# Optimization experiments

Hardware: AMD Instinct MI355X
Metric: run time of the kernel (lower is better)

The kernel has to match this reference:

```python
import jax, jax.numpy as jnp
import numpy as np

N, C, H, K = 4096, 512, 128, 3
NEG = -jnp.inf


def _linear(x, W, b):
    return x @ W.T + b


def _lrelu(x):
    return jnp.where(x > 0, x, 0.01 * x)  # nn.LeakyReLU default slope


def _cos_sim(x, y):
    # torch cal_cos_similarity: xy / (|x| |y|^T), NaN (0/0) -> 0
    xy = x @ y.T
    den = jnp.linalg.norm(x, axis=1, keepdims=True) * jnp.linalg.norm(y, axis=1, keepdims=True).T
    return xy / jnp.where(den == 0, 1.0, den)


def setup_inputs() -> dict:
    key = jax.random.key(0)
    ks = jax.random.split(key, 24)
    x_hidden = jax.random.normal(ks[0], (N, H), jnp.float32)
    cm = (jax.random.uniform(ks[1], (N, C)) < 0.05).astype(jnp.float32)
    # ensure every concept has at least one member stock (no empty concepts)
    cm = cm.at[jnp.arange(C) % N, jnp.arange(C)].set(1.0)
    market_value = jax.random.uniform(ks[2], (N,), jnp.float32, 0.1, 1.0)
    s = 1.0 / np.sqrt(H)
    inp = {"x_hidden": x_hidden, "concept_matrix": cm, "market_value": market_value}
    names = ["ps", "ps_fore", "ps_back", "hs", "hs_fore", "hs_back", "indi"]
    for i, n in enumerate(names):
        inp[f"W_{n}"] = jax.random.uniform(ks[3 + 2 * i], (H, H), jnp.float32, -s, s)
        inp[f"b_{n}"] = jax.random.uniform(ks[4 + 2 * i], (H,), jnp.float32, -s, s)
    inp["W_out"] = jax.random.uniform(ks[20], (1, H), jnp.float32, -s, s)
    inp["b_out"] = jax.random.uniform(ks[21], (1,), jnp.float32, -s, s)
    return inp


def reference(x_hidden, concept_matrix, market_value,
              W_ps, b_ps, W_ps_fore, b_ps_fore, W_ps_back, b_ps_back,
              W_hs, b_hs, W_hs_fore, b_hs_fore, W_hs_back, b_hs_back,
              W_indi, b_indi, W_out, b_out):
    x = x_hidden
    n = x.shape[0]
    # --- predefined-concept (ps) branch ---
    s2c = concept_matrix * market_value[:, None]                     # [N,C]
    s2c_den = s2c.sum(0)[None, :] * concept_matrix + 1.0
    s2c = s2c / s2c_den
    hidden = s2c.T @ x                                               # [C,H]
    valid1 = hidden.sum(1) != 0                                      # row-filter mask
    s2c2 = jax.nn.softmax(x @ hidden.T, axis=0)                      # softmax over stocks
    hidden = (s2c2.T @ x) * valid1[:, None]                          # [C,H]
    c2s = jax.nn.softmax(jnp.where(valid1[None, :], _cos_sim(x, hidden), NEG), axis=1)
    p_shared = _linear(c2s @ hidden, W_ps, b_ps)
    p_back = _linear(p_shared, W_ps_back, b_ps_back)
    out_ps = _lrelu(_linear(p_shared, W_ps_fore, b_ps_fore))
    # --- hidden-concept (hs) branch ---
    h = x - p_back
    hs2c = _cos_sim(h, h)                                            # [N,N]
    diag = jnp.diagonal(hs2c)
    hs2c = hs2c * (1.0 - jnp.eye(n, dtype=h.dtype))
    idx = jax.lax.top_k(hs2c, K)[1]                                  # [N,K]
    mask = jnp.zeros((n, n), h.dtype).at[jnp.arange(n)[:, None], idx].set(1.0)
    hs2c = hs2c * mask
    hs2c = hs2c + jnp.diag((hs2c.sum(0) != 0).astype(h.dtype) * diag)
    hidden2 = hs2c.T @ h                                             # [N,H]
    valid2 = hidden2.sum(1) != 0
    hidden2 = hidden2 * valid2[:, None]
    hc2s = jax.nn.softmax(jnp.where(valid2[None, :], _cos_sim(h, hidden2), NEG), axis=1)
    h_shared = _linear(hc2s @ hidden2, W_hs, b_hs)
    h_back = _linear(h_shared, W_hs_back, b_hs_back)
    out_hs = _lrelu(_linear(h_shared, W_hs_fore, b_hs_fore))
    # --- individual branch ---
    indiv = x - p_back - h_back
    out_indi = _lrelu(_linear(indiv, W_indi, b_indi))
    all_info = out_ps + out_hs + out_indi
    return _linear(all_info, W_out, b_out).squeeze()                 # [N]
```

## Files before the change

### kernel.cpp

```cpp
#include <hip/hip_runtime.h>
#include <hip/hip_fp16.h>
#include <math.h>

#define N 4096
#define C 512
#define H 128
#define PAD 40
#define WP 136
#define FWP 136
#define SP 136

typedef __attribute__((ext_vector_type(8))) short bf16x8;
typedef __attribute__((ext_vector_type(4))) float f32x4;


__device__ inline float wave_reduce_sum(float v) {
#pragma unroll
  for (int m = 32; m; m >>= 1) v += __shfl_xor(v, m);
  return v;
}

__device__ inline float lrelu(float v) { return v > 0.f ? v : 0.01f * v; }

__device__ inline bool better(float v, int j, float w, int k) {
  return (v > w) || (v == w && j < k);
}

__device__ inline void top3_ins(float v, int j, float& v0, int& j0,
                                float& v1, int& j1, float& v2, int& j2) {
  if (better(v, j, v0, j0)) { v2 = v1; j2 = j1; v1 = v0; j1 = j0; v0 = v; j0 = j; }
  else if (better(v, j, v1, j1)) { v2 = v1; j2 = j1; v1 = v; j1 = j; }
  else if (better(v, j, v2, j2)) { v2 = v; j2 = j; }
}

__device__ inline void ins5(float s, int j, float v[5], int jx[5]) {
  if (!better(s, j, v[4], jx[4])) return;
  if (better(s, j, v[0], jx[0])) {
    v[4]=v[3]; jx[4]=jx[3]; v[3]=v[2]; jx[3]=jx[2]; v[2]=v[1]; jx[2]=jx[1];
    v[1]=v[0]; jx[1]=jx[0]; v[0]=s; jx[0]=j;
  } else if (better(s, j, v[1], jx[1])) {
    v[4]=v[3]; jx[4]=jx[3]; v[3]=v[2]; jx[3]=jx[2]; v[2]=v[1]; jx[2]=jx[1];
    v[1]=s; jx[1]=j;
  } else if (better(s, j, v[2], jx[2])) {
    v[4]=v[3]; jx[4]=jx[3]; v[3]=v[2]; jx[3]=jx[2]; v[2]=s; jx[2]=j;
  } else if (better(s, j, v[3], jx[3])) {
    v[4]=v[3]; jx[4]=jx[3]; v[3]=s; jx[3]=j;
  } else {
    v[4]=s; jx[4]=j;
  }
}

__device__ inline unsigned short f2bf(float f) {
  unsigned u = __float_as_uint(f);
  unsigned r = u + 0x7fffu + ((u >> 16) & 1u);
  return (unsigned short)(r >> 16);
}
__device__ inline float bf2f(unsigned short h) {
  return __uint_as_float(((unsigned)h) << 16);
}

__global__ __launch_bounds__(256) void k_split(const float* __restrict__ in,
                                               unsigned short* __restrict__ hi,
                                               unsigned short* __restrict__ lo,
                                               float* __restrict__ nrm) {
  int t = threadIdx.x;
  int idx = (blockIdx.x * 256 + t) * 4;
  float4 v = *(const float4*)&in[idx];
  float vv[4] = {v.x, v.y, v.z, v.w};
  unsigned short h[4], l[4];
  float ss = 0.f;
#pragma unroll
  for (int c = 0; c < 4; c++) {
    ss += vv[c] * vv[c];
    h[c] = f2bf(vv[c]);
    l[c] = f2bf(vv[c] - bf2f(h[c]));
  }
  uint2 ph = {(unsigned)h[0] | ((unsigned)h[1] << 16),
              (unsigned)h[2] | ((unsigned)h[3] << 16)};
  uint2 pl = {(unsigned)l[0] | ((unsigned)l[1] << 16),
              (unsigned)l[2] | ((unsigned)l[3] << 16)};
  *(uint2*)&hi[idx] = ph;
  *(uint2*)&lo[idx] = pl;
  if (nrm) {
#pragma unroll
    for (int m = 16; m; m >>= 1) ss += __shfl_xor(ss, m);
    if ((t & 31) == 0) nrm[idx >> 7] = sqrtf(ss);
  }
}

__global__ __launch_bounds__(256) void k_tsplit(const float* __restrict__ in,
                                                unsigned short* __restrict__ thi,
                                                unsigned short* __restrict__ tlo,
                                                int R) {
  __shared__ float tile[32][132];
  int r0 = blockIdx.x * 32, tid = threadIdx.x;
#pragma unroll
  for (int q = 0; q < 4; q++) {
    int f = q * 256 + tid;
    int row = f >> 5, ch = f & 31;
    *(float4*)&tile[row][ch * 4] = *(const float4*)&in[(size_t)(r0 + row) * 128 + ch * 4];
  }
  __syncthreads();
  int c = tid & 127, half = tid >> 7;
  unsigned short hh[16], ll[16];
#pragma unroll
  for (int rr = 0; rr < 16; rr++) {
    float v = tile[half * 16 + rr][c];
    hh[rr] = f2bf(v);
    ll[rr] = f2bf(v - bf2f(hh[rr]));
  }
  size_t off = (size_t)c * R + r0 + half * 16;
  uint4 ph0 = {(unsigned)hh[0] | ((unsigned)hh[1] << 16), (unsigned)hh[2] | ((unsigned)hh[3] << 16),
               (unsigned)hh[4] | ((unsigned)hh[5] << 16), (unsigned)hh[6] | ((unsigned)hh[7] << 16)};
  uint4 ph1 = {(unsigned)hh[8] | ((unsigned)hh[9] << 16), (unsigned)hh[10] | ((unsigned)hh[11] << 16),
               (unsigned)hh[12] | ((unsigned)hh[13] << 16), (unsigned)hh[14] | ((unsigned)hh[15] << 16)};
  uint4 pl0 = {(unsigned)ll[0] | ((unsigned)ll[1] << 16), (unsigned)ll[2] | ((unsigned)ll[3] << 16),
               (unsigned)ll[4] | ((unsigned)ll[5] << 16), (unsigned)ll[6] | ((unsigned)ll[7] << 16)};
  uint4 pl1 = {(unsigned)ll[8] | ((unsigned)ll[9] << 16), (unsigned)ll[10] | ((unsigned)ll[11] << 16),
               (unsigned)ll[12] | ((unsigned)ll[13] << 16), (unsigned)ll[14] | ((unsigned)ll[15] << 16)};
  *(uint4*)&thi[off] = ph0; *(uint4*)&thi[off + 8] = ph1;
  *(uint4*)&tlo[off] = pl0; *(uint4*)&tlo[off + 8] = pl1;
}


__global__ __launch_bounds__(64) void k_colsum_s2c(
    const float* __restrict__ cm, const float* __restrict__ mv,
    float* __restrict__ colsum_c) {
  int c = blockIdx.x * 64 + threadIdx.x;
  int i0 = blockIdx.y * 256;
  float acc = 0.f;
  for (int i = i0; i < i0 + 256; i++) acc += cm[(size_t)i * C + c] * mv[i];
  atomicAdd(&colsum_c[c], acc);
}

__global__ __launch_bounds__(256) void k_colstats(const float* __restrict__ sc,
                                                  float* __restrict__ colmax,
                                                  float* __restrict__ colsum) {
  __shared__ float red[256];
  int c = blockIdx.x, t = threadIdx.x;
  float v[16];
  float m = -3e38f;
#pragma unroll
  for (int q = 0; q < 16; q++) {
    v[q] = sc[(size_t)(q * 256 + t) * C + c];
    m = fmaxf(m, v[q]);
  }
  red[t] = m; __syncthreads();
  for (int s = 128; s; s >>= 1) { if (t < s) red[t] = fmaxf(red[t], red[t + s]); __syncthreads(); }
  m = red[0]; __syncthreads();
  float sum = 0.f;
#pragma unroll
  for (int q = 0; q < 16; q++) sum += __expf(v[q] - m);
  red[t] = sum; __syncthreads();
  for (int s = 128; s; s >>= 1) { if (t < s) red[t] += red[t + s]; __syncthreads(); }
  if (t == 0) { colmax[c] = m; colsum[c] = red[0]; }
}

__global__ __launch_bounds__(256) void k_cs_softmax(
    const float* __restrict__ sc, const float* __restrict__ xnorm,
    const float* __restrict__ hnorm, const float* __restrict__ valid1,
    unsigned short* __restrict__ cshi, unsigned short* __restrict__ cslo) {
  __shared__ float red[256];
  int i = blockIdx.x, t = threadIdx.x;
  float xn = xnorm[i];
  float r0 = sc[(size_t)i * C + t], r1 = sc[(size_t)i * C + 256 + t];
  float d0 = xn * hnorm[t], d1 = xn * hnorm[256 + t];
  float c0 = r0 / (d0 == 0.f ? 1.f : d0);
  float c1 = r1 / (d1 == 0.f ? 1.f : d1);
  float s0 = (valid1[t] != 0.f) ? c0 : -3e38f;
  float s1 = (valid1[256 + t] != 0.f) ? c1 : -3e38f;
  red[t] = fmaxf(s0, s1); __syncthreads();
  for (int s = 128; s; s >>= 1) { if (t < s) red[t] = fmaxf(red[t], red[t + s]); __syncthreads(); }
  float m = red[0]; __syncthreads();
  float p0 = (s0 > -1e37f) ? __expf(s0 - m) : 0.f;
  float p1 = (s1 > -1e37f) ? __expf(s1 - m) : 0.f;
  red[t] = p0 + p1; __syncthreads();
  for (int s = 128; s; s >>= 1) { if (t < s) red[t] += red[t + s]; __syncthreads(); }
  float inv = 1.f / red[0];
  float a = p0 * inv, b = p1 * inv;
  unsigned short ha = f2bf(a), hb = f2bf(b);
  cshi[(size_t)i * C + t] = ha;
  cslo[(size_t)i * C + t] = f2bf(a - bf2f(ha));
  cshi[(size_t)i * C + 256 + t] = hb;
  cslo[(size_t)i * C + 256 + t] = f2bf(b - bf2f(hb));
}

__global__ __launch_bounds__(64) void k_fin_hidden2(
    const float* __restrict__ h, const float* __restrict__ diagv,
    const float* __restrict__ colsum_m, float* __restrict__ hidden2,
    unsigned short* __restrict__ h2hi, unsigned short* __restrict__ h2lo,
    float* __restrict__ valid2f) {
  int j = blockIdx.x, t = threadIdx.x;
  float add = (colsum_m[j] != 0.f) ? diagv[j] : 0.f;
  float a = hidden2[(size_t)j * H + t] + add * h[(size_t)j * H + t];
  float b = hidden2[(size_t)j * H + 64 + t] + add * h[(size_t)j * H + 64 + t];
  float s = a + b, ss = a * a + b * b;
#pragma unroll
  for (int m = 32; m; m >>= 1) { s += __shfl_xor(s, m); ss += __shfl_xor(ss, m); }
  bool valid = (s != 0.f);
  a = valid ? a : 0.f; b = valid ? b : 0.f;
  hidden2[(size_t)j * H + t] = a;
  hidden2[(size_t)j * H + 64 + t] = b;
  float inv = (valid && ss > 0.f) ? (1.f / sqrtf(ss)) : 1.f;
  float va = a * inv, vb = b * inv;
  unsigned short ha = f2bf(va), hb = f2bf(vb);
  h2hi[(size_t)j * H + t] = ha;
  h2lo[(size_t)j * H + t] = f2bf(va - bf2f(ha));
  h2hi[(size_t)j * H + 64 + t] = hb;
  h2lo[(size_t)j * H + 64 + t] = f2bf(vb - bf2f(hb));
  if (t == 0) valid2f[j] = valid ? 1.f : 0.f;
}

template <int EPI>
__global__ __launch_bounds__(256) void k_mfma_nt(
    const unsigned short* __restrict__ Ahi, const unsigned short* __restrict__ Alo,
    const unsigned short* __restrict__ Bhi, const unsigned short* __restrict__ Blo,
    float* __restrict__ out, float2* __restrict__ cand, int Nn) {
  __shared__ __align__(16) unsigned short sAh[128 * PAD];
  __shared__ __align__(16) unsigned short sAl[128 * PAD];
  __shared__ __align__(16) unsigned short sBh[128 * PAD];
  __shared__ __align__(16) unsigned short sBl[128 * PAD];
  int tid = threadIdx.x;
  int bm = blockIdx.y * 128, bn = blockIdx.x * 128;
  int lane = tid & 63, w = tid >> 6;
  int wm = (w & 1) * 64, wn = (w >> 1) * 64;
  int l15 = lane & 15, quad = lane >> 4;
  f32x4 zero = {0.f, 0.f, 0.f, 0.f};
  f32x4 acc[4][4];
#pragma unroll
  for (int mt = 0; mt < 4; mt++)
#pragma unroll
    for (int nt = 0; nt < 4; nt++) acc[mt][nt] = zero;

  for (int kt = 0; kt < 128; kt += 32) {
#pragma unroll
    for (int q = 0; q < 2; q++) {
      int f = tid * 2 + q;
      int row = f >> 2, ch = f & 3;
      size_t ga = (size_t)(bm + row) * 128 + kt + ch * 8;
      size_t gb = (size_t)(bn + row) * 128 + kt + ch * 8;
      int ls = row * PAD + ch * 8;
      *(uint4*)&sAh[ls] = *(const uint4*)&Ahi[ga];
      *(uint4*)&sAl[ls] = *(const uint4*)&Alo[ga];
      *(uint4*)&sBh[ls] = *(const uint4*)&Bhi[gb];
      *(uint4*)&sBl[ls] = *(const uint4*)&Blo[gb];
    }
    __syncthreads();
    bf16x8 ah[4], al[4], bh[4], bl[4];
#pragma unroll
    for (int t = 0; t < 4; t++) {
      int ar = (wm + t * 16 + l15) * PAD + quad * 8;
      ah[t] = *(const bf16x8*)&sAh[ar];
      al[t] = *(const bf16x8*)&sAl[ar];
      int br = (wn + t * 16 + l15) * PAD + quad * 8;
      bh[t] = *(const bf16x8*)&sBh[br];
      bl[t] = *(const bf16x8*)&sBl[br];
    }
#pragma unroll
    for (int mt = 0; mt < 4; mt++)
#pragma unroll
      for (int nt = 0; nt < 4; nt++) {
        acc[mt][nt] = __builtin_amdgcn_mfma_f32_16x16x32_bf16(ah[mt], bh[nt], acc[mt][nt], 0, 0, 0);
        acc[mt][nt] = __builtin_amdgcn_mfma_f32_16x16x32_bf16(ah[mt], bl[nt], acc[mt][nt], 0, 0, 0);
        acc[mt][nt] = __builtin_amdgcn_mfma_f32_16x16x32_bf16(al[mt], bh[nt], acc[mt][nt], 0, 0, 0);
      }
    __syncthreads();
  }
  if constexpr (EPI == 2) {
    __shared__ __align__(16) unsigned short sS[128 * SP];
#pragma unroll
    for (int mt = 0; mt < 4; mt++)
#pragma unroll
      for (int nt = 0; nt < 4; nt++) {
        int coll = wn + nt * 16 + l15;
#pragma unroll
        for (int rg = 0; rg < 4; rg++) {
          int rowl = wm + mt * 16 + quad * 4 + rg;
          float v = (bm + rowl == bn + coll) ? 0.f : acc[mt][nt][rg];
          sS[rowl * SP + coll] = __half_as_ushort(__float2half(v));
        }
      }
    __syncthreads();
    int r = tid >> 1, hf = tid & 1;
    const unsigned short* rowp = &sS[r * SP + hf * 64];
    int cbase = bn + hf * 64;
    float v5[5] = {-3e38f, -3e38f, -3e38f, -3e38f, -3e38f};
    int j5[5] = {0x7fffffff, 0x7fffffff, 0x7fffffff, 0x7fffffff, 0x7fffffff};
#pragma unroll
    for (int q = 0; q < 8; q++) {
      uint4 p = *(const uint4*)&rowp[q * 8];
      unsigned pk[4] = {p.x, p.y, p.z, p.w};
#pragma unroll
      for (int c2 = 0; c2 < 4; c2++) {
        float e0 = __half2float(__ushort_as_half((unsigned short)(pk[c2] & 0xffffu)));
        float e1 = __half2float(__ushort_as_half((unsigned short)(pk[c2] >> 16)));
        ins5(e0, cbase + q * 8 + c2 * 2, v5, j5);
        ins5(e1, cbase + q * 8 + c2 * 2 + 1, v5, j5);
      }
    }
    int slot = (bn >> 6) + hf;
    float2* cp = &cand[((size_t)(bm + r) * 64 + slot) * 5];
#pragma unroll
    for (int c2 = 0; c2 < 5; c2++) cp[c2] = {v5[c2], __int_as_float(j5[c2])};
  } else {
#pragma unroll
    for (int mt = 0; mt < 4; mt++) {
#pragma unroll
      for (int nt = 0; nt < 4; nt++) {
        int col = bn + wn + nt * 16 + l15;
#pragma unroll
        for (int rg = 0; rg < 4; rg++) {
          int row = bm + wm + mt * 16 + quad * 4 + rg;
          out[(size_t)row * Nn + col] = acc[mt][nt][rg];
        }
      }
    }
  }
}

__global__ __launch_bounds__(256) void k_rowtop2(
    const float2* __restrict__ cand, const float* __restrict__ hhat,
    float* __restrict__ mtv, int* __restrict__ mtj) {
  int i = blockIdx.x * 4 + (threadIdx.x >> 6);
  int lane = threadIdx.x & 63;
  const float2* cr = &cand[(size_t)i * 320];
  float v[5] = {-3e38f, -3e38f, -3e38f, -3e38f, -3e38f};
  int jx[5] = {0x7fffffff, 0x7fffffff, 0x7fffffff, 0x7fffffff, 0x7fffffff};
#pragma unroll
  for (int c = 0; c < 5; c++) {
    float2 p = cr[lane * 5 + c];
    ins5(p.x, __float_as_int(p.y), v, jx);
  }
#pragma unroll
  for (int d = 1; d < 64; d <<= 1) {
    float fv[5]; int fj[5];
#pragma unroll
    for (int c = 0; c < 5; c++) { fv[c] = __shfl_xor(v[c], d); fj[c] = __shfl_xor(jx[c], d); }
#pragma unroll
    for (int c = 0; c < 5; c++) ins5(fv[c], fj[c], v, jx);
  }
  const float* hi = &hhat[(size_t)i * H];
  float b0 = -3e38f, b1 = -3e38f, b2 = -3e38f;
  int q0 = 0, q1 = 0, q2 = 0;
#pragma unroll
  for (int c = 0; c < 5; c++) {
    int j = jx[c];
    float s;
    if (j == i) {
      s = 0.f;
    } else {
      const float* hj = &hhat[(size_t)j * H];
      float p = hi[lane] * hj[lane] + hi[lane + 64] * hj[lane + 64];
      s = wave_reduce_sum(p);
    }
    top3_ins(s, j, b0, q0, b1, q1, b2, q2);
  }
  if (lane == 0) {
    mtv[i * 3 + 0] = b0; mtv[i * 3 + 1] = b1; mtv[i * 3 + 2] = b2;
    mtj[i * 3 + 0] = q0; mtj[i * 3 + 1] = q1; mtj[i * 3 + 2] = q2;
  }
}

__global__ __launch_bounds__(512) void k_flash(
    const unsigned short* __restrict__ Qhi, const unsigned short* __restrict__ Qlo,
    const unsigned short* __restrict__ Khi, const unsigned short* __restrict__ Klo,
    const unsigned short* __restrict__ Vthi, const unsigned short* __restrict__ Vtlo,
    const float* __restrict__ valid2f, float* __restrict__ partialU,
    float* __restrict__ plsum, int KVC) {
  __shared__ __align__(16) unsigned short sQh[128 * FWP];
  __shared__ __align__(16) unsigned short sQl[128 * FWP];
  __shared__ __align__(16) unsigned short sP[128 * FWP];
  __shared__ __align__(16) unsigned short sKh[128 * PAD];
  __shared__ __align__(16) unsigned short sKl[128 * PAD];
  __shared__ __align__(16) unsigned short sVh[128 * PAD];
  __shared__ __align__(16) unsigned short sVl[128 * PAD];
  __shared__ float lsum_s[128];
  int tid = threadIdx.x;
  int z = blockIdx.x;
  int bm = blockIdx.y * 128;
  int j0 = z * KVC;
  int lane = tid & 63, w = tid >> 6;
  int wm = (w & 3) * 32, wn = (w >> 2) * 64;
  int l15 = lane & 15, quad = lane >> 4;
#pragma unroll
  for (int q = 0; q < 4; q++) {
    int f = q * 512 + tid;
    int row = f >> 4, ch = f & 15;
    size_t ga = (size_t)(bm + row) * 128 + ch * 8;
    int ls = row * FWP + ch * 8;
    *(uint4*)&sQh[ls] = *(const uint4*)&Qhi[ga];
    *(uint4*)&sQl[ls] = *(const uint4*)&Qlo[ga];
  }
  if (tid < 128) lsum_s[tid] = 0.f;
  __syncthreads();
  f32x4 zero = {0.f, 0.f, 0.f, 0.f};
  f32x4 uacc[2][4];
#pragma unroll
  for (int mt = 0; mt < 2; mt++)
#pragma unroll
    for (int nt = 0; nt < 4; nt++) uacc[mt][nt] = zero;

  for (int jb = j0; jb < j0 + KVC; jb += 128) {
    float vm[4];
#pragma unroll
    for (int nt = 0; nt < 4; nt++) vm[nt] = valid2f[jb + wn + nt * 16 + l15];
    f32x4 qacc[2][4];
#pragma unroll
    for (int mt = 0; mt < 2; mt++)
#pragma unroll
      for (int nt = 0; nt < 4; nt++) qacc[mt][nt] = zero;
    for (int kt = 0; kt < 128; kt += 32) {
      {
        int row = tid >> 2, ch = tid & 3;
        size_t gb = (size_t)(jb + row) * 128 + kt + ch * 8;
        int ls = row * PAD + ch * 8;
        *(uint4*)&sKh[ls] = *(const uint4*)&Khi[gb];
        *(uint4*)&sKl[ls] = *(const uint4*)&Klo[gb];
      }
      __syncthreads();
      bf16x8 ah[2], al[2], bh[4], bl[4];
#pragma unroll
      for (int t = 0; t < 2; t++) {
        int ar = (wm + t * 16 + l15) * FWP + kt + quad * 8;
        ah[t] = *(const bf16x8*)&sQh[ar];
        al[t] = *(const bf16x8*)&sQl[ar];
      }
#pragma unroll
      for (int t = 0; t < 4; t++) {
        int br = (wn + t * 16 + l15) * PAD + quad * 8;
        bh[t] = *(const bf16x8*)&sKh[br];
        bl[t] = *(const bf16x8*)&sKl[br];
      }
#pragma unroll
      for (int mt = 0; mt < 2; mt++)
#pragma unroll
        for (int nt = 0; nt < 4; nt++) {
          qacc[mt][nt] = __builtin_amdgcn_mfma_f32_16x16x32_bf16(ah[mt], bh[nt], qacc[mt][nt], 0, 0, 0);
          qacc[mt][nt] = __builtin_amdgcn_mfma_f32_16x16x32_bf16(ah[mt], bl[nt], qacc[mt][nt], 0, 0, 0);
          qacc[mt][nt] = __builtin_amdgcn_mfma_f32_16x16x32_bf16(al[mt], bh[nt], qacc[mt][nt], 0, 0, 0);
        }
      __syncthreads();
    }
#pragma unroll
    for (int mt = 0; mt < 2; mt++) {
#pragma unroll
      for (int rg = 0; rg < 4; rg++) {
        int row = wm + mt * 16 + quad * 4 + rg;
        float rs = 0.f;
#pragma unroll
        for (int nt = 0; nt < 4; nt++) {
          float e = (vm[nt] != 0.f) ? __expf(qacc[mt][nt][rg] - 1.f) : 0.f;
          rs += e;
          sP[row * FWP + wn + nt * 16 + l15] = f2bf(e);
        }
#pragma unroll
        for (int d = 1; d < 16; d <<= 1) rs += __shfl_xor(rs, d);
        if (l15 == 0) atomicAdd(&lsum_s[row], rs);
      }
    }
    for (int kt = 0; kt < 128; kt += 32) {
      {
        int row = tid >> 2, ch = tid & 3;
        size_t gv = (size_t)row * N + jb + kt + ch * 8;
        int ls = row * PAD + ch * 8;
        *(uint4*)&sVh[ls] = *(const uint4*)&Vthi[gv];
        *(uint4*)&sVl[ls] = *(const uint4*)&Vtlo[gv];
      }
      __syncthreads();
      bf16x8 pa[2], vh[4], vl[4];
#pragma unroll
      for (int t = 0; t < 2; t++) {
        int ar = (wm + t * 16 + l15) * FWP + kt + quad * 8;
        pa[t] = *(const bf16x8*)&sP[ar];
      }
#pragma unroll
      for (int t = 0; t < 4; t++) {
        int br = (wn + t * 16 + l15) * PAD + quad * 8;
        vh[t] = *(const bf16x8*)&sVh[br];
        vl[t] = *(const bf16x8*)&sVl[br];
      }
#pragma unroll
      for (int mt = 0; mt < 2; mt++)
#pragma unroll
        for (int nt = 0; nt < 4; nt++) {
          uacc[mt][nt] = __builtin_amdgcn_mfma_f32_16x16x32_bf16(pa[mt], vh[nt], uacc[mt][nt], 0, 0, 0);
          uacc[mt][nt] = __builtin_amdgcn_mfma_f32_16x16x32_bf16(pa[mt], vl[nt], uacc[mt][nt], 0, 0, 0);
        }
      __syncthreads();
    }
  }
  float* pU = partialU + (size_t)z * N * 128;
#pragma unroll
  for (int mt = 0; mt < 2; mt++)
#pragma unroll
    for (int nt = 0; nt < 4; nt++) {
      int col = wn + nt * 16 + l15;
#pragma unroll
      for (int rg = 0; rg < 4; rg++) {
        int row = bm + wm + mt * 16 + quad * 4 + rg;
        pU[(size_t)row * 128 + col] = uacc[mt][nt][rg];
      }
    }
  if (tid < 128) plsum[(size_t)z * N + bm + tid] = lsum_s[tid];
}

__global__ __launch_bounds__(256) void k_mfma_kn(
    const unsigned short* __restrict__ Ahi, const unsigned short* __restrict__ Alo,
    const unsigned short* __restrict__ Bthi, const unsigned short* __restrict__ Btlo,
    float* __restrict__ partial, int lda, int KC) {
  __shared__ __align__(16) unsigned short sAh[128 * PAD];
  __shared__ __align__(16) unsigned short sAl[128 * PAD];
  __shared__ __align__(16) unsigned short sBh[128 * PAD];
  __shared__ __align__(16) unsigned short sBl[128 * PAD];
  int tid = threadIdx.x;
  int bm = blockIdx.y * 128;
  int k0 = blockIdx.z * KC;
  int lane = tid & 63, w = tid >> 6;
  int wm = (w & 1) * 64, wn = (w >> 1) * 64;
  int l15 = lane & 15, quad = lane >> 4;
  f32x4 zero = {0.f, 0.f, 0.f, 0.f};
  f32x4 acc[4][4];
#pragma unroll
  for (int mt = 0; mt < 4; mt++)
#pragma unroll
    for (int nt = 0; nt < 4; nt++) acc[mt][nt] = zero;

  for (int kt = 0; kt < KC; kt += 32) {
#pragma unroll
    for (int q = 0; q < 2; q++) {
      int f = tid * 2 + q;
      int row = f >> 2, ch = f & 3;
      size_t ga = (size_t)(bm + row) * lda + k0 + kt + ch * 8;
      size_t gb = (size_t)row * lda + k0 + kt + ch * 8;
      int ls = row * PAD + ch * 8;
      *(uint4*)&sAh[ls] = *(const uint4*)&Ahi[ga];
      *(uint4*)&sAl[ls] = *(const uint4*)&Alo[ga];
      *(uint4*)&sBh[ls] = *(const uint4*)&Bthi[gb];
      *(uint4*)&sBl[ls] = *(const uint4*)&Btlo[gb];
    }
    __syncthreads();
    bf16x8 ah[4], al[4], bh[4], bl[4];
#pragma unroll
    for (int t = 0; t < 4; t++) {
      int ar = (wm + t * 16 + l15) * PAD + quad * 8;
      ah[t] = *(const bf16x8*)&sAh[ar];
      al[t] = *(const bf16x8*)&sAl[ar];
      int br = (wn + t * 16 + l15) * PAD + quad * 8;
      bh[t] = *(const bf16x8*)&sBh[br];
      bl[t] = *(const bf16x8*)&sBl[br];
    }
#pragma unroll
    for (int mt = 0; mt < 4; mt++)
#pragma unroll
      for (int nt = 0; nt < 4; nt++) {
        acc[mt][nt] = __builtin_amdgcn_mfma_f32_16x16x32_bf16(ah[mt], bh[nt], acc[mt][nt], 0, 0, 0);
        acc[mt][nt] = __builtin_amdgcn_mfma_f32_16x16x32_bf16(ah[mt], bl[nt], acc[mt][nt], 0, 0, 0);
        acc[mt][nt] = __builtin_amdgcn_mfma_f32_16x16x32_bf16(al[mt], bh[nt], acc[mt][nt], 0, 0, 0);
      }
    __syncthreads();
  }
  float* pp = partial + (size_t)blockIdx.z * N * 128;
#pragma unroll
  for (int mt = 0; mt < 4; mt++)
#pragma unroll
    for (int nt = 0; nt < 4; nt++) {
      int col = wn + nt * 16 + l15;
#pragma unroll
      for (int rg = 0; rg < 4; rg++) {
        int row = bm + wm + mt * 16 + quad * 4 + rg;
        pp[(size_t)row * 128 + col] = acc[mt][nt][rg];
      }
    }
}

template <int AMODE>
__global__ __launch_bounds__(256) void k_mfma_genA(
    const float* __restrict__ P, const float* __restrict__ mv,
    const float* __restrict__ col1, const float* __restrict__ col2,
    const unsigned short* __restrict__ Bthi, const unsigned short* __restrict__ Btlo,
    float* __restrict__ partial, int KC) {
  __shared__ __align__(16) unsigned short sAh[128 * PAD];
  __shared__ __align__(16) unsigned short sAl[128 * PAD];
  __shared__ __align__(16) unsigned short sBh[128 * PAD];
  __shared__ __align__(16) unsigned short sBl[128 * PAD];
  int tid = threadIdx.x;
  int bm = blockIdx.y * 128;
  int k0 = blockIdx.z * KC;
  int lane = tid & 63, w = tid >> 6;
  int wm = (w & 1) * 64, wn = (w >> 1) * 64;
  int l15 = lane & 15, quad = lane >> 4;
  f32x4 zero = {0.f, 0.f, 0.f, 0.f};
  f32x4 acc[4][4];
#pragma unroll
  for (int mt = 0; mt < 4; mt++)
#pragma unroll
    for (int nt = 0; nt < 4; nt++) acc[mt][nt] = zero;

  for (int kt = 0; kt < KC; kt += 32) {
    int kr = tid >> 3;
    int mc = (tid & 7) * 16;
    int k = k0 + kt + kr;
    float mvk = (AMODE == 1) ? mv[k] : 0.f;
#pragma unroll
    for (int q = 0; q < 4; q++) {
      int m0 = mc + q * 4;
      float4 pv = *(const float4*)&P[(size_t)k * C + bm + m0];
      float4 c1 = *(const float4*)&col1[bm + m0];
      float wv[4];
      if (AMODE == 1) {
        wv[0] = pv.x * mvk / (c1.x * pv.x + 1.f);
        wv[1] = pv.y * mvk / (c1.y * pv.y + 1.f);
        wv[2] = pv.z * mvk / (c1.z * pv.z + 1.f);
        wv[3] = pv.w * mvk / (c1.w * pv.w + 1.f);
      } else {
        float4 c2 = *(const float4*)&col2[bm + m0];
        wv[0] = __expf(pv.x - c1.x) / c2.x;
        wv[1] = __expf(pv.y - c1.y) / c2.y;
        wv[2] = __expf(pv.z - c1.z) / c2.z;
        wv[3] = __expf(pv.w - c1.w) / c2.w;
      }
#pragma unroll
      for (int j = 0; j < 4; j++) {
        unsigned short hh = f2bf(wv[j]);
        sAh[(m0 + j) * PAD + kr] = hh;
        sAl[(m0 + j) * PAD + kr] = f2bf(wv[j] - bf2f(hh));
      }
    }
#pragma unroll
    for (int q = 0; q < 2; q++) {
      int f = q * 256 + tid;
      int row = f >> 2, ch = f & 3;
      size_t gb = (size_t)row * N + k0 + kt + ch * 8;
      int ls = row * PAD + ch * 8;
// ... 150 lines not shown
  __shared__ __align__(16) unsigned short sAh[32 * WP];
  __shared__ __align__(16) unsigned short sAl[32 * WP];
  __shared__ __align__(16) float sF[32][132];
  int tid = threadIdx.x;
  int bm = blockIdx.x * 32;
  int lane = tid & 63, w = tid >> 6;
  int rt = (w & 1) * 16, ch2 = (w >> 1) * 64;
  int l15 = lane & 15, quad = lane >> 4;
  f32x4 zero = {0.f, 0.f, 0.f, 0.f};
  f32x4 acc[4];

  {
    int row = tid >> 3, c0 = (tid & 7) * 16;
    const float* src = &A[(size_t)(bm + row) * 128 + c0];
#pragma unroll
    for (int q = 0; q < 4; q++) {
      float4 v = *(const float4*)&src[q * 4];
      float vv[4] = {v.x, v.y, v.z, v.w};
#pragma unroll
      for (int c = 0; c < 4; c++) {
        unsigned short hh = f2bf(vv[c]);
        sAh[row * WP + c0 + q * 4 + c] = hh;
        sAl[row * WP + c0 + q * 4 + c] = f2bf(vv[c] - bf2f(hh));
      }
    }
  }
  LOAD_W(W_ps);
  __syncthreads();
  GEMM32(acc);
  __syncthreads();
#pragma unroll
  for (int nt = 0; nt < 4; nt++) {
    int col = ch2 + nt * 16 + l15;
    float bv = b_ps[col];
#pragma unroll
    for (int rg = 0; rg < 4; rg++) {
      int row = rt + quad * 4 + rg;
      float v = acc[nt][rg] + bv;
      unsigned short hh = f2bf(v);
      sAh[row * WP + col] = hh;
      sAl[row * WP + col] = f2bf(v - bf2f(hh));
    }
  }
  LOAD_W(W_psb);
  __syncthreads();
  GEMM32(acc);
#pragma unroll
  for (int nt = 0; nt < 4; nt++) {
    int col = ch2 + nt * 16 + l15;
    float bv = b_psb[col];
#pragma unroll
    for (int rg = 0; rg < 4; rg++) {
      int row = rt + quad * 4 + rg;
      size_t off = (size_t)(bm + row) * 128 + col;
      float hv = x[off] - (acc[nt][rg] + bv);
      hbuf[off] = hv;
      sF[row][col] = hv;
    }
  }
  __syncthreads();
  {
    int row = tid >> 3, c0 = (tid & 7) * 16;
    float hv16[16];
    float ssp = 0.f;
#pragma unroll
    for (int q = 0; q < 16; q++) {
      float v = sF[row][c0 + q];
      hv16[q] = v;
      ssp += v * v;
    }
    ssp += __shfl_xor(ssp, 1);
    ssp += __shfl_xor(ssp, 2);
    ssp += __shfl_xor(ssp, 4);
    float ss = ssp;
    float hn = sqrtf(ss);
    float den = hn * hn;
    float dg = (den == 0.f) ? 0.f : ss / den;
    float inv = (ss > 0.f) ? (1.f / hn) : 1.f;
    size_t base = (size_t)(bm + row) * H + c0;
    float va16[16];
    unsigned short hh16[16], ll16[16];
#pragma unroll
    for (int q = 0; q < 16; q++) {
      va16[q] = hv16[q] * inv;
      hh16[q] = f2bf(va16[q]);
      ll16[q] = f2bf(va16[q] - bf2f(hh16[q]));
    }
#pragma unroll
    for (int q4 = 0; q4 < 4; q4++) {
      float4 fv = {va16[q4 * 4], va16[q4 * 4 + 1], va16[q4 * 4 + 2], va16[q4 * 4 + 3]};
      *(float4*)&hhat[base + q4 * 4] = fv;
    }
    uint4 ph0 = {(unsigned)hh16[0] | ((unsigned)hh16[1] << 16), (unsigned)hh16[2] | ((unsigned)hh16[3] << 16),
                 (unsigned)hh16[4] | ((unsigned)hh16[5] << 16), (unsigned)hh16[6] | ((unsigned)hh16[7] << 16)};
    uint4 ph1 = {(unsigned)hh16[8] | ((unsigned)hh16[9] << 16), (unsigned)hh16[10] | ((unsigned)hh16[11] << 16),
                 (unsigned)hh16[12] | ((unsigned)hh16[13] << 16), (unsigned)hh16[14] | ((unsigned)hh16[15] << 16)};
    uint4 pl0 = {(unsigned)ll16[0] | ((unsigned)ll16[1] << 16), (unsigned)ll16[2] | ((unsigned)ll16[3] << 16),
                 (unsigned)ll16[4] | ((unsigned)ll16[5] << 16), (unsigned)ll16[6] | ((unsigned)ll16[7] << 16)};
    uint4 pl1 = {(unsigned)ll16[8] | ((unsigned)ll16[9] << 16), (unsigned)ll16[10] | ((unsigned)ll16[11] << 16),
                 (unsigned)ll16[12] | ((unsigned)ll16[13] << 16), (unsigned)ll16[14] | ((unsigned)ll16[15] << 16)};
    *(uint4*)&hhi[base] = ph0; *(uint4*)&hhi[base + 8] = ph1;
    *(uint4*)&hlo[base] = pl0; *(uint4*)&hlo[base + 8] = pl1;
    if ((tid & 7) == 0) diagv[bm + row] = dg;
  }
  LOAD_W(W_psf);
  __syncthreads();
  GEMM32(acc);
#pragma unroll
  for (int nt = 0; nt < 4; nt++) {
    int col = ch2 + nt * 16 + l15;
    float bv = b_psf[col];
#pragma unroll
    for (int rg = 0; rg < 4; rg++) {
      int row = rt + quad * 4 + rg;
      size_t off = (size_t)(bm + row) * 128 + col;
      all_info[off] = lrelu(acc[nt][rg] + bv);
    }
  }
}

__global__ __launch_bounds__(256) void k_hs_tail(
    const float* __restrict__ A, const float* __restrict__ hbuf,
    const float* __restrict__ all_info,
    const float* __restrict__ W_hs, const float* __restrict__ b_hs,
    const float* __restrict__ W_hsf, const float* __restrict__ b_hsf,
    const float* __restrict__ W_hsb, const float* __restrict__ b_hsb,
    const float* __restrict__ W_in, const float* __restrict__ b_in,
    const float* __restrict__ W_out, const float* __restrict__ b_out,
    float* __restrict__ out) {
  __shared__ __align__(16) unsigned short sWh[128 * WP];
  __shared__ __align__(16) unsigned short sWl[128 * WP];
  __shared__ __align__(16) unsigned short sAh[32 * WP];
  __shared__ __align__(16) unsigned short sAl[32 * WP];
  __shared__ __align__(16) float sF[32][132];
  int tid = threadIdx.x;
  int bm = blockIdx.x * 32;
  int lane = tid & 63, w = tid >> 6;
  int rt = (w & 1) * 16, ch2 = (w >> 1) * 64;
  int l15 = lane & 15, quad = lane >> 4;
  f32x4 zero = {0.f, 0.f, 0.f, 0.f};
  f32x4 acc[4];
  float allv[4][4];

  {
    int row = tid >> 3, c0 = (tid & 7) * 16;
    const float* src = &A[(size_t)(bm + row) * 128 + c0];
#pragma unroll
    for (int q = 0; q < 4; q++) {
      float4 v = *(const float4*)&src[q * 4];
      float vv[4] = {v.x, v.y, v.z, v.w};
#pragma unroll
      for (int c = 0; c < 4; c++) {
        unsigned short hh = f2bf(vv[c]);
        sAh[row * WP + c0 + q * 4 + c] = hh;
        sAl[row * WP + c0 + q * 4 + c] = f2bf(vv[c] - bf2f(hh));
      }
    }
  }
  LOAD_W(W_hs);
  __syncthreads();
  GEMM32(acc);
  __syncthreads();
#pragma unroll
  for (int nt = 0; nt < 4; nt++) {
    int col = ch2 + nt * 16 + l15;
    float bv = b_hs[col];
#pragma unroll
    for (int rg = 0; rg < 4; rg++) {
      int row = rt + quad * 4 + rg;
      float v = acc[nt][rg] + bv;
      unsigned short hh = f2bf(v);
      sAh[row * WP + col] = hh;
      sAl[row * WP + col] = f2bf(v - bf2f(hh));
    }
  }
  LOAD_W(W_hsf);
  __syncthreads();
  GEMM32(acc);
#pragma unroll
  for (int nt = 0; nt < 4; nt++) {
    int col = ch2 + nt * 16 + l15;
    float bv = b_hsf[col];
#pragma unroll
    for (int rg = 0; rg < 4; rg++) {
      int row = rt + quad * 4 + rg;
      size_t off = (size_t)(bm + row) * 128 + col;
      allv[nt][rg] = all_info[off] + lrelu(acc[nt][rg] + bv);
    }
  }
  __syncthreads();
  LOAD_W(W_hsb);
  __syncthreads();
  GEMM32(acc);
  float iv[4][4];
#pragma unroll
  for (int nt = 0; nt < 4; nt++) {
    int col = ch2 + nt * 16 + l15;
    float bv = b_hsb[col];
#pragma unroll
    for (int rg = 0; rg < 4; rg++) {
      int row = rt + quad * 4 + rg;
      size_t off = (size_t)(bm + row) * 128 + col;
      iv[nt][rg] = hbuf[off] - (acc[nt][rg] + bv);
    }
  }
  __syncthreads();
#pragma unroll
  for (int nt = 0; nt < 4; nt++) {
    int col = ch2 + nt * 16 + l15;
#pragma unroll
    for (int rg = 0; rg < 4; rg++) {
      int row = rt + quad * 4 + rg;
      unsigned short hh = f2bf(iv[nt][rg]);
      sAh[row * WP + col] = hh;
      sAl[row * WP + col] = f2bf(iv[nt][rg] - bf2f(hh));
    }
  }
  LOAD_W(W_in);
  __syncthreads();
  GEMM32(acc);
#pragma unroll
  for (int nt = 0; nt < 4; nt++) {
    int col = ch2 + nt * 16 + l15;
    float bv = b_in[col];
#pragma unroll
    for (int rg = 0; rg < 4; rg++) {
      int row = rt + quad * 4 + rg;
      allv[nt][rg] += lrelu(acc[nt][rg] + bv);
      sF[row][col] = allv[nt][rg];
    }
  }
  __syncthreads();
  {
    int row = tid >> 3, c0 = (tid & 7) * 16;
    float s = 0.f;
#pragma unroll
    for (int q = 0; q < 16; q++) s += sF[row][c0 + q] * W_out[c0 + q];
    s += __shfl_xor(s, 1);
    s += __shfl_xor(s, 2);
    s += __shfl_xor(s, 4);
    if ((tid & 7) == 0) out[bm + row] = s + b_out[0];
  }
}


extern "C" void kernel_launch(void* const* d_in, const int* in_sizes, int n_in,
                              void* d_out, int out_size, void* d_ws, size_t ws_size,
                              hipStream_t stream) {
  (void)in_sizes; (void)n_in; (void)out_size; (void)ws_size;
  const float* x   = (const float*)d_in[0];
  const float* cm  = (const float*)d_in[1];
  const float* mv  = (const float*)d_in[2];
  const float* W_ps = (const float*)d_in[3],  *b_ps = (const float*)d_in[4];
  const float* W_psf = (const float*)d_in[5], *b_psf = (const float*)d_in[6];
  const float* W_psb = (const float*)d_in[7], *b_psb = (const float*)d_in[8];
  const float* W_hs = (const float*)d_in[9],  *b_hs = (const float*)d_in[10];
  const float* W_hsf = (const float*)d_in[11], *b_hsf = (const float*)d_in[12];
  const float* W_hsb = (const float*)d_in[13], *b_hsb = (const float*)d_in[14];
  const float* W_in = (const float*)d_in[15], *b_in = (const float*)d_in[16];
  const float* W_out = (const float*)d_in[17], *b_out = (const float*)d_in[18];
  float* out = (float*)d_out;

  float* W = (float*)d_ws;
  size_t o = 0;
  auto alloc = [&](size_t n) { float* p = W + o; o += n; return p; };
  float* colsum_c = alloc(C);
  float* colmax   = alloc(C);
  float* colsumexp= alloc(C);
  float* valid1   = alloc(C);
  float* hnorm_ps = alloc(C);
  float* xnorm    = alloc(N);
  float* diagv    = alloc(N);
  float* colsum_m = alloc(N);
  float* valid2f  = alloc(N);
  float* plsum    = alloc((size_t)8 * N);
  float* mtv      = alloc(3 * N);
  int*   mtj      = (int*)alloc(3 * N);
  float* hidden1  = alloc((size_t)C * H);
  float* hidden_ps= alloc((size_t)C * H);
  float* scores   = alloc((size_t)N * C);
  float* ps_pre   = alloc((size_t)N * H);
  float* all_info = alloc((size_t)N * H);
  float* hbuf     = alloc((size_t)N * H);
  float* hhat     = alloc((size_t)N * H);
  float* hidden2  = alloc((size_t)N * H);
  unsigned short* xhi    = (unsigned short*)alloc((size_t)N * H / 2);
  unsigned short* xlo    = (unsigned short*)alloc((size_t)N * H / 2);
  unsigned short* hhathi = (unsigned short*)alloc((size_t)N * H / 2);
  unsigned short* hhatlo = (unsigned short*)alloc((size_t)N * H / 2);
  unsigned short* h2hi   = (unsigned short*)alloc((size_t)N * H / 2);
  unsigned short* h2lo   = (unsigned short*)alloc((size_t)N * H / 2);
  unsigned short* h1hi   = (unsigned short*)alloc((size_t)C * H / 2);
  unsigned short* h1lo   = (unsigned short*)alloc((size_t)C * H / 2);
  unsigned short* hpshi  = (unsigned short*)alloc((size_t)C * H / 2);
  unsigned short* hpslo  = (unsigned short*)alloc((size_t)C * H / 2);
  unsigned short* cshi   = (unsigned short*)alloc((size_t)N * C / 2);
  unsigned short* cslo   = (unsigned short*)alloc((size_t)N * C / 2);
  unsigned short* hpst_hi= (unsigned short*)alloc((size_t)H * C / 2);
  unsigned short* hpst_lo= (unsigned short*)alloc((size_t)H * C / 2);
  unsigned short* h2t_hi = (unsigned short*)alloc((size_t)H * N / 2);
  unsigned short* h2t_lo = (unsigned short*)alloc((size_t)H * N / 2);
  unsigned short* xt_hi  = (unsigned short*)alloc((size_t)H * N / 2);
  unsigned short* xt_lo  = (unsigned short*)alloc((size_t)H * N / 2);
  float2* cand    = (float2*)alloc((size_t)N * 64 * 5 * 2);
  float* partial  = W + o;
  const int Z = 8;

  hipMemsetAsync(colsum_c, 0, C * sizeof(float), stream);
  hipMemsetAsync(colsum_m, 0, N * sizeof(float), stream);
  hipMemsetAsync(hidden2, 0, (size_t)N * H * sizeof(float), stream);

  dim3 blk(256);
  k_split<<<dim3(N * H / 1024), blk, 0, stream>>>(x, xhi, xlo, xnorm);
  k_tsplit<<<dim3(N / 32), blk, 0, stream>>>(x, xt_hi, xt_lo, N);
  k_colsum_s2c<<<dim3(C / 64, 16), dim3(64), 0, stream>>>(cm, mv, colsum_c);
  k_mfma_genA<1><<<dim3(1, C / 128, 32), blk, 0, stream>>>(
      cm, mv, colsum_c, nullptr, xt_hi, xt_lo, partial, N / 32);
  k_reduce<<<dim3(C * H / 4 / 256), blk, 0, stream>>>(
      partial, hidden1, 32, (size_t)C * H, (size_t)C * H / 4, nullptr, nullptr,
      h1hi, h1lo, nullptr, valid1);
  k_mfma_nt<0><<<dim3(C / 128, N / 128), blk, 0, stream>>>(
      xhi, xlo, h1hi, h1lo, scores, nullptr, C);
  k_colstats<<<dim3(C), blk, 0, stream>>>(scores, colmax, colsumexp);
  k_mfma_genA<2><<<dim3(1, C / 128, 32), blk, 0, stream>>>(
      scores, nullptr, colmax, colsumexp, xt_hi, xt_lo, partial, N / 32);
  k_reduce<<<dim3(C * H / 4 / 256), blk, 0, stream>>>(
      partial, hidden_ps, 32, (size_t)C * H, (size_t)C * H / 4, valid1, nullptr,
      hpshi, hpslo, hnorm_ps, nullptr);
  k_mfma_nt<0><<<dim3(C / 128, N / 128), blk, 0, stream>>>(
      xhi, xlo, hpshi, hpslo, scores, nullptr, C);
  k_cs_softmax<<<dim3(N), blk, 0, stream>>>(scores, xnorm, hnorm_ps, valid1,
                                            cshi, cslo);
  k_tsplit<<<dim3(C / 32), blk, 0, stream>>>(hidden_ps, hpst_hi, hpst_lo, C);
  k_mfma_kn<<<dim3(1, N / 128, 4), blk, 0, stream>>>(
      cshi, cslo, hpst_hi, hpst_lo, partial, C, C / 4);
  k_reduce<<<dim3(N * H / 4 / 256), blk, 0, stream>>>(
      partial, ps_pre, 4, (size_t)N * H, (size_t)N * H / 4, nullptr, nullptr,
      nullptr, nullptr, nullptr, nullptr);
  k_ps_tail<<<dim3(N / 32), blk, 0, stream>>>(
      ps_pre, x, W_ps, b_ps, W_psb, b_psb, W_psf, b_psf,
      hbuf, hhat, hhathi, hhatlo, diagv, all_info);
  k_mfma_nt<2><<<dim3(N / 128, N / 128), blk, 0, stream>>>(
      hhathi, hhatlo, hhathi, hhatlo, nullptr, cand, N);
  k_rowtop2<<<dim3(N / 4), blk, 0, stream>>>(cand, hhat, mtv, mtj);
  k_scatter<<<dim3(N / 4), blk, 0, stream>>>(mtv, mtj, hbuf, hidden2, colsum_m);
  k_fin_hidden2<<<dim3(N), dim3(64), 0, stream>>>(hbuf, diagv, colsum_m, hidden2,
                                                  h2hi, h2lo, valid2f);
  k_tsplit<<<dim3(N / 32), blk, 0, stream>>>(hidden2, h2t_hi, h2t_lo, N);
  k_flash<<<dim3(Z, N / 128), dim3(512), 0, stream>>>(
      hhathi, hhatlo, h2hi, h2lo, h2t_hi, h2t_lo, valid2f, partial, plsum,
      N / Z);
  k_reduce<<<dim3(N * H / 4 / 256), blk, 0, stream>>>(
      partial, ps_pre, Z, (size_t)N * H, (size_t)N * H / 4, nullptr, plsum,
      nullptr, nullptr, nullptr, nullptr);
  k_hs_tail<<<dim3(N / 32), blk, 0, stream>>>(
      ps_pre, hbuf, all_info, W_hs, b_hs, W_hsf, b_hsf, W_hsb, b_hsb,
      W_in, b_in, W_out, b_out, out);
}
```

Before: 372.4 us.

## Split similarity top-k kernel into 512-thread blocks with finer candidate slots

```diff
diff --git a/kernel.cpp b/kernel.cpp
--- a/kernel.cpp
+++ b/kernel.cpp
@@ -211,11 +211,10 @@
   if (t == 0) valid2f[j] = valid ? 1.f : 0.f;
 }
 
-template <int EPI>
 __global__ __launch_bounds__(256) void k_mfma_nt(
     const unsigned short* __restrict__ Ahi, const unsigned short* __restrict__ Alo,
     const unsigned short* __restrict__ Bhi, const unsigned short* __restrict__ Blo,
-    float* __restrict__ out, float2* __restrict__ cand, int Nn) {
+    float* __restrict__ out, int Nn) {
   __shared__ __align__(16) unsigned short sAh[128 * PAD];
   __shared__ __align__(16) unsigned short sAl[128 * PAD];
   __shared__ __align__(16) unsigned short sBh[128 * PAD];
@@ -266,56 +265,109 @@
       }
     __syncthreads();
   }
-  if constexpr (EPI == 2) {
-    __shared__ __align__(16) unsigned short sS[128 * SP];
-#pragma unroll
-    for (int mt = 0; mt < 4; mt++)
+#pragma unroll
+  for (int mt = 0; mt < 4; mt++) {
+#pragma unroll
+    for (int nt = 0; nt < 4; nt++) {
+      int col = bn + wn + nt * 16 + l15;
+#pragma unroll
+      for (int rg = 0; rg < 4; rg++) {
+        int row = bm + wm + mt * 16 + quad * 4 + rg;
+        out[(size_t)row * Nn + col] = acc[mt][nt][rg];
+      }
+    }
+  }
+}
+
+__global__ __launch_bounds__(512) void k_snt(
+    const unsigned short* __restrict__ Ahi, const unsigned short* __restrict__ Alo,
+    float2* __restrict__ cand) {
+  __shared__ __align__(16) unsigned short sAh[128 * PAD];
+  __shared__ __align__(16) unsigned short sAl[128 * PAD];
+  __shared__ __align__(16) unsigned short sBh[128 * PAD];
+  __shared__ __align__(16) unsigned short sBl[128 * PAD];
+  __shared__ __align__(16) unsigned short sS[128 * SP];
+  int tid = threadIdx.x;
+  int bm = blockIdx.y * 128, bn = blockIdx.x * 128;
+  int lane = tid & 63, w = tid >> 6;
+  int wm = (w & 3) * 32, wn = (w >> 2) * 64;
+  int l15 = lane & 15, quad = lane >> 4;
+  f32x4 zero = {0.f, 0.f, 0.f, 0.f};
+  f32x4 acc[2][4];
+#pragma unroll
+  for (int mt = 0; mt < 2; mt++)
+#pragma unroll
+    for (int nt = 0; nt < 4; nt++) acc[mt][nt] = zero;
+
+  for (int kt = 0; kt < 128; kt += 32) {
+    {
+      int row = tid >> 2, ch = tid & 3;
+      size_t ga = (size_t)(bm + row) * 128 + kt + ch * 8;
+      size_t gb = (size_t)(bn + row) * 128 + kt + ch * 8;
+      int ls = row * PAD + ch * 8;
+      *(uint4*)&sAh[ls] = *(const uint4*)&Ahi[ga];
+      *(uint4*)&sAl[ls] = *(const uint4*)&Alo[ga];
+      *(uint4*)&sBh[ls] = *(const uint4*)&Ahi[gb];
+      *(uint4*)&sBl[ls] = *(const uint4*)&Alo[gb];
+    }
+    __syncthreads();
+    bf16x8 ah[2], al[2], bh[4], bl[4];
+#pragma unroll
+    for (int t = 0; t < 2; t++) {
+      int ar = (wm + t * 16 + l15) * PAD + quad * 8;
+      ah[t] = *(const bf16x8*)&sAh[ar];
+      al[t] = *(const bf16x8*)&sAl[ar];
+    }
+#pragma unroll
+    for (int t = 0; t < 4; t++) {
+      int br = (wn + t * 16 + l15) * PAD + quad * 8;
+      bh[t] = *(const bf16x8*)&sBh[br];
+      bl[t] = *(const bf16x8*)&sBl[br];
+    }
+#pragma unroll
+    for (int mt = 0; mt < 2; mt++)
 #pragma unroll
       for (int nt = 0; nt < 4; nt++) {
-        int coll = wn + nt * 16 + l15;
-#pragma unroll
-        for (int rg = 0; rg < 4; rg++) {
-          int rowl = wm + mt * 16 + quad * 4 + rg;
-          float v = (bm + rowl == bn + coll) ? 0.f : acc[mt][nt][rg];
-          sS[rowl * SP + coll] = __half_as_ushort(__float2half(v));
-        }
+        acc[mt][nt] = __builtin_amdgcn_mfma_f32_16x16x32_bf16(ah[mt], bh[nt], acc[mt][nt], 0, 0, 0);
+        acc[mt][nt] = __builtin_amdgcn_mfma_f32_16x16x32_bf16(ah[mt], bl[nt], acc[mt][nt], 0, 0, 0);
+        acc[mt][nt] = __builtin_amdgcn_mfma_f32_16x16x32_bf16(al[mt], bh[nt], acc[mt][nt], 0, 0, 0);
       }
     __syncthreads();
-    int r = tid >> 1, hf = tid & 1;
-    const unsigned short* rowp = &sS[r * SP + hf * 64];
-    int cbase = bn + hf * 64;
-    float v5[5] = {-3e38f, -3e38f, -3e38f, -3e38f, -3e38f};
-    int j5[5] = {0x7fffffff, 0x7fffffff, 0x7fffffff, 0x7fffffff, 0x7fffffff};
-#pragma unroll
-    for (int q = 0; q < 8; q++) {
-      uint4 p = *(const uint4*)&rowp[q * 8];
-      unsigned pk[4] = {p.x, p.y, p.z, p.w};
-#pragma unroll
-      for (int c2 = 0; c2 < 4; c2++) {
-        float e0 = __half2float(__ushort_as_half((unsigned short)(pk[c2] & 0xffffu)));
-        float e1 = __half2float(__ushort_as_half((unsigned short)(pk[c2] >> 16)));
-        ins5(e0, cbase + q * 8 + c2 * 2, v5, j5);
-        ins5(e1, cbase + q * 8 + c2 * 2 + 1, v5, j5);
-      }
-    }
-    int slot = (bn >> 6) + hf;
-    float2* cp = &cand[((size_t)(bm + r) * 64 + slot) * 5];
-#pragma unroll
-    for (int c2 = 0; c2 < 5; c2++) cp[c2] = {v5[c2], __int_as_float(j5[c2])};
-  } else {
-#pragma unroll
-    for (int mt = 0; mt < 4; mt++) {
-#pragma unroll
-      for (int nt = 0; nt < 4; nt++) {
-        int col = bn + wn + nt * 16 + l15;
-#pragma unroll
-        for (int rg = 0; rg < 4; rg++) {
-          int row = bm + wm + mt * 16 + quad * 4 + rg;
-          out[(size_t)row * Nn + col] = acc[mt][nt][rg];
-        }
-      }
-    }
-  }
+  }
+#pragma unroll
+  for (int mt = 0; mt < 2; mt++)
+#pragma unroll
+    for (int nt = 0; nt < 4; nt++) {
+      int coll = wn + nt * 16 + l15;
+#pragma unroll
+      for (int rg = 0; rg < 4; rg++) {
+        int rowl = wm + mt * 16 + quad * 4 + rg;
+        float v = (bm + rowl == bn + coll) ? 0.f : acc[mt][nt][rg];
+        sS[rowl * SP + coll] = __half_as_ushort(__float2half(v));
+      }
+    }
+  __syncthreads();
+  int r = tid >> 2, qf = tid & 3;
+  const unsigned short* rowp = &sS[r * SP + qf * 32];
+  int cbase = bn + qf * 32;
+  float v5[5] = {-3e38f, -3e38f, -3e38f, -3e38f, -3e38f};
+  int j5[5] = {0x7fffffff, 0x7fffffff, 0x7fffffff, 0x7fffffff, 0x7fffffff};
+#pragma unroll
+  for (int q = 0; q < 4; q++) {
+    uint4 p = *(const uint4*)&rowp[q * 8];
+    unsigned pk[4] = {p.x, p.y, p.z, p.w};
+#pragma unroll
+    for (int c2 = 0; c2 < 4; c2++) {
+      float e0 = __half2float(__ushort_as_half((unsigned short)(pk[c2] & 0xffffu)));
+      float e1 = __half2float(__ushort_as_half((unsigned short)(pk[c2] >> 16)));
+      ins5(e0, cbase + q * 8 + c2 * 2, v5, j5);
+      ins5(e1, cbase + q * 8 + c2 * 2 + 1, v5, j5);
+    }
+  }
+  int slot = (bn >> 5) + qf;
+  float2* cp = &cand[((size_t)(bm + r) * 128 + slot) * 5];
+#pragma unroll
+  for (int c2 = 0; c2 < 5; c2++) cp[c2] = {v5[c2], __int_as_float(j5[c2])};
 }
 
 __global__ __launch_bounds__(256) void k_rowtop2(
@@ -323,12 +375,12 @@
     float* __restrict__ mtv, int* __restrict__ mtj) {
   int i = blockIdx.x * 4 + (threadIdx.x >> 6);
   int lane = threadIdx.x & 63;
-  const float2* cr = &cand[(size_t)i * 320];
+  const float2* cr = &cand[(size_t)i * 640];
   float v[5] = {-3e38f, -3e38f, -3e38f, -3e38f, -3e38f};
   int jx[5] = {0x7fffffff, 0x7fffffff, 0x7fffffff, 0x7fffffff, 0x7fffffff};
 #pragma unroll
-  for (int c = 0; c < 5; c++) {
-    float2 p = cr[lane * 5 + c];
+  for (int c = 0; c < 10; c++) {
+    float2 p = cr[lane * 10 + c];
     ins5(p.x, __float_as_int(p.y), v, jx);
   }
 #pragma unroll
@@ -1085,9 +1137,10 @@
   unsigned short* h2t_lo = (unsigned short*)alloc((size_t)H * N / 2);
   unsigned short* xt_hi  = (unsigned short*)alloc((size_t)H * N / 2);
   unsigned short* xt_lo  = (unsigned short*)alloc((size_t)H * N / 2);
-  float2* cand    = (float2*)alloc((size_t)N * 64 * 5 * 2);
+  float2* cand    = (float2*)alloc((size_t)N * 128 * 5 * 2);
   float* partial  = W + o;
   const int Z = 8;
+  const int ZG = 64;
 
   hipMemsetAsync(colsum_c, 0, C * sizeof(float), stream);
   hipMemsetAsync(colsum_m, 0, N * sizeof(float), stream);
@@ -1097,21 +1150,21 @@
   k_split<<<dim3(N * H / 1024), blk, 0, stream>>>(x, xhi, xlo, xnorm);
   k_tsplit<<<dim3(N / 32), blk, 0, stream>>>(x, xt_hi, xt_lo, N);
   k_colsum_s2c<<<dim3(C / 64, 16), dim3(64), 0, stream>>>(cm, mv, colsum_c);
-  k_mfma_genA<1><<<dim3(1, C / 128, 32), blk, 0, stream>>>(
-      cm, mv, colsum_c, nullptr, xt_hi, xt_lo, partial, N / 32);
+  k_mfma_genA<1><<<dim3(1, C / 128, ZG), blk, 0, stream>>>(
+      cm, mv, colsum_c, nullptr, xt_hi, xt_lo, partial, N / ZG);
   k_reduce<<<dim3(C * H / 4 / 256), blk, 0, stream>>>(
-      partial, hidden1, 32, (size_t)C * H, (size_t)C * H / 4, nullptr, nullptr,
+      partial, hidden1, ZG, (size_t)C * H, (size_t)C * H / 4, nullptr, nullptr,
       h1hi, h1lo, nullptr, valid1);
-  k_mfma_nt<0><<<dim3(C / 128, N / 128), blk, 0, stream>>>(
-      xhi, xlo, h1hi, h1lo, scores, nullptr, C);
+  k_mfma_nt<<<dim3(C / 128, N / 128), blk, 0, stream>>>(
+      xhi, xlo, h1hi, h1lo, scores, C);
   k_colstats<<<dim3(C), blk, 0, stream>>>(scores, colmax, colsumexp);
-  k_mfma_genA<2><<<dim3(1, C / 128, 32), blk, 0, stream>>>(
-      scores, nullptr, colmax, colsumexp, xt_hi, xt_lo, partial, N / 32);
+  k_mfma_genA<2><<<dim3(1, C / 128, ZG), blk, 0, stream>>>(
+      scores, nullptr, colmax, colsumexp, xt_hi, xt_lo, partial, N / ZG);
   k_reduce<<<dim3(C * H / 4 / 256), blk, 0, stream>>>(
-      partial, hidden_ps, 32, (size_t)C * H, (size_t)C * H / 4, valid1, nullptr,
+      partial, hidden_ps, ZG, (size_t)C * H, (size_t)C * H / 4, valid1, nullptr,
       hpshi, hpslo, hnorm_ps, nullptr);
-  k_mfma_nt<0><<<dim3(C / 128, N / 128), blk, 0, stream>>>(
-      xhi, xlo, hpshi, hpslo, scores, nullptr, C);
+  k_mfma_nt<<<dim3(C / 128, N / 128), blk, 0, stream>>>(
+      xhi, xlo, hpshi, hpslo, scores, C);
   k_cs_softmax<<<dim3(N), blk, 0, stream>>>(scores, xnorm, hnorm_ps, valid1,
                                             cshi, cslo);
   k_tsplit<<<dim3(C / 32), blk, 0, stream>>>(hidden_ps, hpst_hi, hpst_lo, C);
@@ -1123,8 +1176,8 @@
   k_ps_tail<<<dim3(N / 32), blk, 0, stream>>>(
       ps_pre, x, W_ps, b_ps, W_psb, b_psb, W_psf, b_psf,
       hbuf, hhat, hhathi, hhatlo, diagv, all_info);
-  k_mfma_nt<2><<<dim3(N / 128, N / 128), blk, 0, stream>>>(
-      hhathi, hhatlo, hhathi, hhatlo, nullptr, cand, N);
+  k_snt<<<dim3(N / 128, N / 128), dim3(512), 0, stream>>>(
+      hhathi, hhatlo, cand);
   k_rowtop2<<<dim3(N / 4), blk, 0, stream>>>(cand, hhat, mtv, mtj);
   k_scatter<<<dim3(N / 4), blk, 0, stream>>>(mtv, mtj, hbuf, hidden2, colsum_m);
   k_fin_hidden2<<<dim3(N), dim3(64), 0, stream>>>(hbuf, diagv, colsum_m, hidden2,
```

After: 374.6 us. No clear change (+0.6%).
